# Kernel tuning notes

Hardware: AMD Instinct MI355X
Metric: run time of the kernel (lower is better)

## Reference

```python
import jax, jax.numpy as jnp
import numpy as np

N = 131072
D = 64
K = 1024
COMMITMENT_COST = 0.25


def setup_inputs() -> dict:
    key = jax.random.key(0)
    k1, k2 = jax.random.split(key)
    inputs = jax.random.normal(k1, (N, D), dtype=jnp.float32)
    # nn.Embedding weight initialized uniform(-1/K, 1/K)
    codebook = jax.random.uniform(k2, (K, D), dtype=jnp.float32,
                                  minval=-1.0 / K, maxval=1.0 / K)
    return {"inputs": inputs, "codebook": codebook}


def reference(inputs, codebook):
    # distances[n,k] = ||x_n||^2 + ||e_k||^2 - 2 x_n . e_k   (squared L2)
    distances = (jnp.sum(inputs ** 2, axis=1, keepdims=True)
                 + jnp.sum(codebook ** 2, axis=1)
                 - 2.0 * jnp.matmul(inputs, codebook.T))          # [N, K]
    encoding_indices = jnp.argmin(distances, axis=1)               # [N]
    # one-hot scatter + matmul in the original == direct gather
    quantized = codebook[encoding_indices]                         # [N, D]

    e_latent_loss = jnp.mean((jax.lax.stop_gradient(quantized) - inputs) ** 2)
    q_latent_loss = jnp.mean((quantized - jax.lax.stop_gradient(inputs)) ** 2)
    loss = q_latent_loss + COMMITMENT_COST * e_latent_loss

    # straight-through estimator
    quantized_st = inputs + jax.lax.stop_gradient(quantized - inputs)
    return loss, quantized_st, encoding_indices
```

## Files before the change

### kernel.cpp

```cpp
#include <hip/hip_runtime.h>

#define NN 131072
#define DD 64
#define KK 1024

typedef __attribute__((ext_vector_type(8))) short short8v;
typedef __attribute__((ext_vector_type(4))) float float4v;
typedef __attribute__((ext_vector_type(4))) int int4v;

#define MFMA(a, b, c) __builtin_amdgcn_mfma_f32_16x16x32_bf16(a, b, c, 0, 0, 0)

__device__ __forceinline__ unsigned int umin32(unsigned int a, unsigned int b) { return a < b ? a : b; }
__device__ __forceinline__ unsigned int umax32(unsigned int a, unsigned int b) { return a > b ? a : b; }

__device__ __forceinline__ unsigned int packu(float u, int kk) {
    int b = __builtin_bit_cast(int, u);
    unsigned int key = (unsigned int)(b ^ ((b >> 31) | 0x80000000));
    return (key & 0xFFFFFC00u) | (unsigned int)kk;
}

#define PINS3(t0, t1, t2, p)                                   \
    { unsigned int _x0 = umax32(t0, p); t0 = umin32(t0, p);    \
      unsigned int _x1 = umax32(t1, _x0); t1 = umin32(t1, _x0);\
      t2 = umin32(t2, _x1); }

__device__ __forceinline__ float np_sumsq64(const float* v) {
    float r[8];
#pragma unroll
    for (int j = 0; j < 8; ++j) r[j] = __fmul_rn(v[j], v[j]);
#pragma unroll
    for (int i = 8; i < 64; i += 8) {
#pragma unroll
        for (int j = 0; j < 8; ++j)
            r[j] = __fadd_rn(r[j], __fmul_rn(v[i + j], v[i + j]));
    }
    return __fadd_rn(__fadd_rn(__fadd_rn(r[0], r[1]), __fadd_rn(r[2], r[3])),
                     __fadd_rn(__fadd_rn(r[4], r[5]), __fadd_rn(r[6], r[7])));
}

__device__ __forceinline__ void bf16split(float v, unsigned short& hb, unsigned short& lb) {
    unsigned int u = __builtin_bit_cast(unsigned int, v);
    unsigned int h = (u + 0x7FFFu + ((u >> 16) & 1u)) >> 16;
    float hf = __builtin_bit_cast(float, h << 16);
    float lo = __fsub_rn(v, hf);
    unsigned int ul = __builtin_bit_cast(unsigned int, lo);
    unsigned int lo16 = (ul + 0x7FFFu + ((ul >> 16) & 1u)) >> 16;
    hb = (unsigned short)h;
    lb = (unsigned short)lo16;
}

__global__ void vq_prep(const float* __restrict__ cb, unsigned short* __restrict__ cbh,
                        unsigned short* __restrict__ cbl, float* __restrict__ se) {
    int k = blockIdx.x * 256 + threadIdx.x;
    if (k >= KK) return;
    float v[DD];
    const float4* p = (const float4*)(cb + (size_t)k * DD);
#pragma unroll
    for (int i = 0; i < 16; ++i) {
        float4 q = p[i];
        v[4 * i + 0] = q.x; v[4 * i + 1] = q.y; v[4 * i + 2] = q.z; v[4 * i + 3] = q.w;
    }
    se[k] = np_sumsq64(v);
    short8v* oh = (short8v*)(cbh + (size_t)k * DD);
    short8v* ol = (short8v*)(cbl + (size_t)k * DD);
#pragma unroll
    for (int q = 0; q < 8; ++q) {
        short8v hq, lq;
#pragma unroll
        for (int e = 0; e < 8; ++e) {
            unsigned short hb, lb;
            bf16split(v[q * 8 + e], hb, lb);
            hq[e] = (short)hb; lq[e] = (short)lb;
        }
        oh[q] = hq; ol[q] = lq;
    }
}

union SMem {
    struct { unsigned short xh[128 * 64]; unsigned short xl[128 * 64]; } x;
    struct { unsigned short bh[2][64 * 64]; unsigned short bl[2][64 * 64]; } b;
};

__global__ __launch_bounds__(256, 4)
void vq_main(const float* __restrict__ x, const float* __restrict__ cb,
             const unsigned short* __restrict__ cbh, const unsigned short* __restrict__ cbl,
             const float* __restrict__ se, float* __restrict__ qout,
             float* __restrict__ idxf, double* __restrict__ acc) {
    __shared__ SMem sm;
    __shared__ float ses[KK];
    __shared__ float wls[4];

    const int tid = threadIdx.x;
    const int rowBase = blockIdx.x * 128;
    const int l = tid & 63;
    const int w = tid >> 6;
    const int col = l & 15;
    const int g = l >> 4;

    int4v rbh[2], rbl[2];
    const int be_ = tid >> 2;
    const int bq_ = (tid & 3) * 2;
#define LOAD_TILE(tt)                                                              \
    { const unsigned short* ph = cbh + ((size_t)((tt) * 64 + be_) * 64) + (tid & 3) * 16; \
      const unsigned short* pl = cbl + ((size_t)((tt) * 64 + be_) * 64) + (tid & 3) * 16; \
      rbh[0] = *(const int4v*)(ph); rbh[1] = *(const int4v*)(ph + 8);              \
      rbl[0] = *(const int4v*)(pl); rbl[1] = *(const int4v*)(pl + 8); }
#define WRITE_TILE(bufi)                                                           \
    { int4v* dh = (int4v*)sm.b.bh[bufi]; int4v* dl = (int4v*)sm.b.bl[bufi];        \
      dh[be_ * 8 + (bq_ ^ (be_ & 7))] = rbh[0];                                    \
      dh[be_ * 8 + ((bq_ + 1) ^ (be_ & 7))] = rbh[1];                              \
      dl[be_ * 8 + (bq_ ^ (be_ & 7))] = rbl[0];                                    \
      dl[be_ * 8 + ((bq_ + 1) ^ (be_ & 7))] = rbl[1]; }

    ((float4v*)ses)[tid] = ((const float4v*)se)[tid];

    {
        int row = tid >> 1, db = (tid & 1) * 32;
        const float* xr = x + (size_t)(rowBase + row) * 64 + db;
#pragma unroll
        for (int jj = 0; jj < 4; ++jj) {
            float4 v0 = ((const float4*)xr)[2 * jj];
            float4 v1 = ((const float4*)xr)[2 * jj + 1];
            float vv[8] = {v0.x, v0.y, v0.z, v0.w, v1.x, v1.y, v1.z, v1.w};
            short8v hq, lq;
#pragma unroll
            for (int e = 0; e < 8; ++e) {
                unsigned short hb, lb;
                bf16split(vv[e], hb, lb);
                hq[e] = (short)hb; lq[e] = (short)lb;
            }
            int q = (tid & 1) * 4 + jj;
            int slot = row * 8 + (q ^ (row & 7));
            ((short8v*)sm.x.xh)[slot] = hq;
            ((short8v*)sm.x.xl)[slot] = lq;
        }
    }
    LOAD_TILE(0);
    __syncthreads();

    short8v ah0s0, ah1s0, al0s0, al1s0, ah0s1, ah1s1, al0s1, al1s1;
    {
        int r0 = w * 32 + col;
        int r1 = r0 + 16;
        ah0s0 = ((short8v*)sm.x.xh)[r0 * 8 + ((0 + g) ^ (r0 & 7))];
        ah1s0 = ((short8v*)sm.x.xh)[r0 * 8 + ((4 + g) ^ (r0 & 7))];
        al0s0 = ((short8v*)sm.x.xl)[r0 * 8 + ((0 + g) ^ (r0 & 7))];
        al1s0 = ((short8v*)sm.x.xl)[r0 * 8 + ((4 + g) ^ (r0 & 7))];
        ah0s1 = ((short8v*)sm.x.xh)[r1 * 8 + ((0 + g) ^ (r1 & 7))];
        ah1s1 = ((short8v*)sm.x.xh)[r1 * 8 + ((4 + g) ^ (r1 & 7))];
        al0s1 = ((short8v*)sm.x.xl)[r1 * 8 + ((0 + g) ^ (r1 & 7))];
        al1s1 = ((short8v*)sm.x.xl)[r1 * 8 + ((4 + g) ^ (r1 & 7))];
    }
    __syncthreads();

    WRITE_TILE(0);
    LOAD_TILE(1);
    __syncthreads();

    unsigned int k0[8], k1[8], k2[8];
#pragma unroll
    for (int s = 0; s < 8; ++s) { k0[s] = 0xFFFFFFFFu; k1[s] = 0xFFFFFFFFu; k2[s] = 0xFFFFFFFFu; }

    for (int t = 0; t < 16; ++t) {
        if (t < 15) {
            WRITE_TILE((t + 1) & 1);
            if (t < 14) LOAD_TILE(t + 2);
        }
        const unsigned short* bhB = sm.b.bh[t & 1];
        const unsigned short* blB = sm.b.bl[t & 1];
#pragma unroll
        for (int c = 0; c < 4; ++c) {
            int ec = c * 16 + col;
            int be = ec * 8, sw = ec & 7;
            short8v bh0 = ((const short8v*)bhB)[be + ((0 + g) ^ sw)];
            short8v bh1 = ((const short8v*)bhB)[be + ((4 + g) ^ sw)];
            short8v bl0 = ((const short8v*)blB)[be + ((0 + g) ^ sw)];
            short8v bl1 = ((const short8v*)blB)[be + ((4 + g) ^ sw)];
            float sek = ses[t * 64 + ec];
            float4v acc0 = {0.f, 0.f, 0.f, 0.f}, acc1 = {0.f, 0.f, 0.f, 0.f};
            acc0 = MFMA(ah0s0, bh0, acc0);
            acc0 = MFMA(ah1s0, bh1, acc0);
            acc0 = MFMA(al0s0, bh0, acc0);
            acc0 = MFMA(al1s0, bh1, acc0);
            acc0 = MFMA(ah0s0, bl0, acc0);
            acc0 = MFMA(ah1s0, bl1, acc0);
            acc1 = MFMA(ah0s1, bh0, acc1);
            acc1 = MFMA(ah1s1, bh1, acc1);
            acc1 = MFMA(al0s1, bh0, acc1);
            acc1 = MFMA(al1s1, bh1, acc1);
            acc1 = MFMA(ah0s1, bl0, acc1);
            acc1 = MFMA(ah1s1, bl1, acc1);
            int kk = t * 64 + ec;
#pragma unroll
            for (int r = 0; r < 4; ++r) {
                unsigned int p0 = packu(fmaf(-2.f, acc0[r], sek), kk);
                PINS3(k0[r], k1[r], k2[r], p0);
                unsigned int p1 = packu(fmaf(-2.f, acc1[r], sek), kk);
                PINS3(k0[4 + r], k1[4 + r], k2[4 + r], p1);
            }
        }
        __syncthreads();
    }

#pragma unroll
    for (int s = 0; s < 8; ++s) {
#pragma unroll
        for (int m = 1; m < 16; m <<= 1) {
            unsigned int o0 = __shfl_xor(k0[s], m);
            unsigned int o1 = __shfl_xor(k1[s], m);
            unsigned int o2 = __shfl_xor(k2[s], m);
            PINS3(k0[s], k1[s], k2[s], o0);
            { unsigned int x1 = umax32(k1[s], o1); k1[s] = umin32(k1[s], o1);
              k2[s] = umin32(k2[s], x1); }
            k2[s] = umin32(k2[s], o2);
        }
    }

    float lossLocal = 0.f;
    const int rr = (l & 15) >> 2;
    const int j = l & 3;
    const int jj = (j == 3) ? 0 : j;
#pragma unroll
    for (int s = 0; s < 2; ++s) {
        unsigned int ckk = k0[s * 4];
#pragma unroll
        for (int r_ = 0; r_ < 4; ++r_) {
            if (rr == r_) {
                if (jj == 0) ckk = k0[s * 4 + r_];
                else if (jj == 1) ckk = k1[s * 4 + r_];
                else ckk = k2[s * 4 + r_];
            }
        }
        int ck = (int)(ckk & 1023u);
        int rowg = rowBase + w * 32 + s * 16 + g * 4 + rr;
        const float4* xr = (const float4*)(x + (size_t)rowg * 64);
        const float4* er = (const float4*)(cb + (size_t)ck * 64);
        float dot = 0.f;
        float rs0 = 0.f, rs1 = 0.f, rs2 = 0.f, rs3 = 0.f, rs4 = 0.f, rs5 = 0.f, rs6 = 0.f, rs7 = 0.f;
#pragma unroll
        for (int i = 0; i < 16; ++i) {
            float4 a4 = xr[i], e4 = er[i];
            dot = fmaf(a4.x, e4.x, dot);
            dot = fmaf(a4.y, e4.y, dot);
            dot = fmaf(a4.z, e4.z, dot);
            dot = fmaf(a4.w, e4.w, dot);
            if ((i & 1) == 0) {
                rs0 = __fadd_rn(rs0, __fmul_rn(a4.x, a4.x));
                rs1 = __fadd_rn(rs1, __fmul_rn(a4.y, a4.y));
                rs2 = __fadd_rn(rs2, __fmul_rn(a4.z, a4.z));
                rs3 = __fadd_rn(rs3, __fmul_rn(a4.w, a4.w));
            } else {
                rs4 = __fadd_rn(rs4, __fmul_rn(a4.x, a4.x));
                rs5 = __fadd_rn(rs5, __fmul_rn(a4.y, a4.y));
                rs6 = __fadd_rn(rs6, __fmul_rn(a4.z, a4.z));
                rs7 = __fadd_rn(rs7, __fmul_rn(a4.w, a4.w));
            }
        }
        float sa = __fadd_rn(__fadd_rn(__fadd_rn(rs0, rs1), __fadd_rn(rs2, rs3)),
                             __fadd_rn(__fadd_rn(rs4, rs5), __fadd_rn(rs6, rs7)));
        float qd = __fsub_rn(__fadd_rn(sa, ses[ck]), __fmul_rn(2.f, dot));
#pragma unroll
        for (int m = 1; m < 4; m <<= 1) {
            float oq = __shfl_xor(qd, m);
            int ok = __shfl_xor(ck, m);
            if (oq < qd || (oq == qd && ok < ck)) { qd = oq; ck = ok; }
        }
        if (j == 0) idxf[rowg] = (float)ck;
        const float4* qr = (const float4*)(cb + (size_t)ck * 64);
        float* orow = qout + (size_t)rowg * 64;
#pragma unroll
        for (int p = 0; p < 4; ++p) {
            int iq = j * 4 + p;
            float4 xv = xr[iq];
            float4 qv = qr[iq];
            float dx = __fsub_rn(qv.x, xv.x);
            float dy = __fsub_rn(qv.y, xv.y);
            float dz = __fsub_rn(qv.z, xv.z);
            float dw = __fsub_rn(qv.w, xv.w);
            float4 o;
            o.x = __fadd_rn(xv.x, dx);
            o.y = __fadd_rn(xv.y, dy);
            o.z = __fadd_rn(xv.z, dz);
            o.w = __fadd_rn(xv.w, dw);
            ((float4*)orow)[iq] = o;
            lossLocal = fmaf(dx, dx, lossLocal);
            lossLocal = fmaf(dy, dy, lossLocal);
            lossLocal = fmaf(dz, dz, lossLocal);
            lossLocal = fmaf(dw, dw, lossLocal);
        }
    }
#pragma unroll
    for (int m = 1; m < 64; m <<= 1) lossLocal += __shfl_xor(lossLocal, m);
    if (l == 0) wls[w] = lossLocal;
    __syncthreads();
    if (tid == 0) atomicAdd(acc, (double)(wls[0] + wls[1] + wls[2] + wls[3]));
}

__global__ void vq_loss(const double* __restrict__ acc, float* __restrict__ out) {
    out[0] = (float)(acc[0] * 1.25 / (double)((size_t)NN * DD));
}

extern "C" void kernel_launch(void* const* d_in, const int* in_sizes, int n_in,
                              void* d_out, int out_size, void* d_ws, size_t ws_size,
                              hipStream_t stream) {
    const float* x = (const float*)d_in[0];
    const float* cb = (const float*)d_in[1];
    float* out = (float*)d_out;

    double* acc = (double*)d_ws;
    float* se = (float*)((char*)d_ws + 64);
    unsigned short* cbh = (unsigned short*)((char*)d_ws + 8192);
    unsigned short* cbl = (unsigned short*)((char*)d_ws + 8192 + 131072);

    hipMemsetAsync(d_ws, 0, 64, stream);

    vq_prep<<<4, 256, 0, stream>>>(cb, cbh, cbl, se);
    vq_main<<<NN / 128, 256, 0, stream>>>(x, cb, cbh, cbl, se,
                                          out + 1, out + 1 + (size_t)NN * DD, acc);
    vq_loss<<<1, 1, 0, stream>>>(acc, out);
}
```

Before: 195.4 us.

## Fold codebook norm into MFMA, fuse loss kernel, align output stores

The codebook is pre-scaled by -2 and its squared norm is split into bf16 hi/lo, which an extra MFMA with a ones vector adds into the accumulators. This removes the per-element fmaf in the argmin epilogue. The separate loss kernel is replaced by a last-block-done counter inside the main kernel, saving one launch. Output stores are shifted so the float4 writes line up with the out+1 offset, and the exact norm is recomputed from fp32 in the refine step. The cost is an extra MFMA per tile and some precision risk in the bf16-split norm.

```diff
diff --git a/kernel.cpp b/kernel.cpp
--- a/kernel.cpp
+++ b/kernel.cpp
@@ -50,8 +50,8 @@
 }
 
 __global__ void vq_prep(const float* __restrict__ cb, unsigned short* __restrict__ cbh,
-                        unsigned short* __restrict__ cbl, float* __restrict__ se) {
-    int k = blockIdx.x * 256 + threadIdx.x;
+                        unsigned short* __restrict__ cbl, unsigned int* __restrict__ sehl) {
+    int k = blockIdx.x * 64 + threadIdx.x;
     if (k >= KK) return;
     float v[DD];
     const float4* p = (const float4*)(cb + (size_t)k * DD);
@@ -60,7 +60,10 @@
         float4 q = p[i];
         v[4 * i + 0] = q.x; v[4 * i + 1] = q.y; v[4 * i + 2] = q.z; v[4 * i + 3] = q.w;
     }
-    se[k] = np_sumsq64(v);
+    float se = np_sumsq64(v);
+    unsigned short sh, sl;
+    bf16split(se, sh, sl);
+    sehl[k] = (unsigned int)sh | ((unsigned int)sl << 16);
     short8v* oh = (short8v*)(cbh + (size_t)k * DD);
     short8v* ol = (short8v*)(cbl + (size_t)k * DD);
 #pragma unroll
@@ -69,7 +72,7 @@
 #pragma unroll
         for (int e = 0; e < 8; ++e) {
             unsigned short hb, lb;
-            bf16split(v[q * 8 + e], hb, lb);
+            bf16split(-2.0f * v[q * 8 + e], hb, lb);
             hq[e] = (short)hb; lq[e] = (short)lb;
         }
         oh[q] = hq; ol[q] = lq;
@@ -84,11 +87,14 @@
 __global__ __launch_bounds__(256, 4)
 void vq_main(const float* __restrict__ x, const float* __restrict__ cb,
              const unsigned short* __restrict__ cbh, const unsigned short* __restrict__ cbl,
-             const float* __restrict__ se, float* __restrict__ qout,
-             float* __restrict__ idxf, double* __restrict__ acc) {
+             const unsigned int* __restrict__ sehl, float* __restrict__ out,
+             double* __restrict__ acc, unsigned int* __restrict__ cnt) {
     __shared__ SMem sm;
-    __shared__ float ses[KK];
+    __shared__ unsigned int sehls[KK];
     __shared__ float wls[4];
+
+    float* qout = out + 1;
+    float* idxf = out + 1 + (size_t)NN * DD;
 
     const int tid = threadIdx.x;
     const int rowBase = blockIdx.x * 128;
@@ -112,7 +118,7 @@
       dl[be_ * 8 + (bq_ ^ (be_ & 7))] = rbl[0];                                    \
       dl[be_ * 8 + ((bq_ + 1) ^ (be_ & 7))] = rbl[1]; }
 
-    ((float4v*)ses)[tid] = ((const float4v*)se)[tid];
+    ((int4v*)sehls)[tid] = ((const int4v*)sehl)[tid];
 
     {
         int row = tid >> 1, db = (tid & 1) * 32;
@@ -157,6 +163,10 @@
     LOAD_TILE(1);
     __syncthreads();
 
+    const short8v onesA = __builtin_bit_cast(short8v,
+        (int4v){(g == 0) ? (int)0x3F803F80 : 0, 0, 0, 0});
+    const float4v zero4 = {0.f, 0.f, 0.f, 0.f};
+
     unsigned int k0[8], k1[8], k2[8];
 #pragma unroll
     for (int s = 0; s < 8; ++s) { k0[s] = 0xFFFFFFFFu; k1[s] = 0xFFFFFFFFu; k2[s] = 0xFFFFFFFFu; }
@@ -176,8 +186,11 @@
             short8v bh1 = ((const short8v*)bhB)[be + ((4 + g) ^ sw)];
             short8v bl0 = ((const short8v*)blB)[be + ((0 + g) ^ sw)];
             short8v bl1 = ((const short8v*)blB)[be + ((4 + g) ^ sw)];
-            float sek = ses[t * 64 + ec];
-            float4v acc0 = {0.f, 0.f, 0.f, 0.f}, acc1 = {0.f, 0.f, 0.f, 0.f};
+            unsigned int sv = sehls[t * 64 + ec];
+            short8v sf = __builtin_bit_cast(short8v,
+                (int4v){(g == 0) ? (int)sv : 0, 0, 0, 0});
+            float4v seAcc = MFMA(onesA, sf, zero4);
+            float4v acc0 = seAcc, acc1 = seAcc;
             acc0 = MFMA(ah0s0, bh0, acc0);
             acc0 = MFMA(ah1s0, bh1, acc0);
             acc0 = MFMA(al0s0, bh0, acc0);
@@ -193,9 +206,9 @@
             int kk = t * 64 + ec;
 #pragma unroll
             for (int r = 0; r < 4; ++r) {
-                unsigned int p0 = packu(fmaf(-2.f, acc0[r], sek), kk);
+                unsigned int p0 = packu(acc0[r], kk);
                 PINS3(k0[r], k1[r], k2[r], p0);
-                unsigned int p1 = packu(fmaf(-2.f, acc1[r], sek), kk);
+                unsigned int p1 = packu(acc1[r], kk);
                 PINS3(k0[4 + r], k1[4 + r], k2[4 + r], p1);
             }
         }
@@ -237,6 +250,7 @@
         const float4* er = (const float4*)(cb + (size_t)ck * 64);
         float dot = 0.f;
         float rs0 = 0.f, rs1 = 0.f, rs2 = 0.f, rs3 = 0.f, rs4 = 0.f, rs5 = 0.f, rs6 = 0.f, rs7 = 0.f;
+        float es0 = 0.f, es1 = 0.f, es2 = 0.f, es3 = 0.f, es4 = 0.f, es5 = 0.f, es6 = 0.f, es7 = 0.f;
 #pragma unroll
         for (int i = 0; i < 16; ++i) {
             float4 a4 = xr[i], e4 = er[i];
@@ -249,16 +263,26 @@
                 rs1 = __fadd_rn(rs1, __fmul_rn(a4.y, a4.y));
                 rs2 = __fadd_rn(rs2, __fmul_rn(a4.z, a4.z));
                 rs3 = __fadd_rn(rs3, __fmul_rn(a4.w, a4.w));
+                es0 = __fadd_rn(es0, __fmul_rn(e4.x, e4.x));
+                es1 = __fadd_rn(es1, __fmul_rn(e4.y, e4.y));
+                es2 = __fadd_rn(es2, __fmul_rn(e4.z, e4.z));
+                es3 = __fadd_rn(es3, __fmul_rn(e4.w, e4.w));
             } else {
                 rs4 = __fadd_rn(rs4, __fmul_rn(a4.x, a4.x));
                 rs5 = __fadd_rn(rs5, __fmul_rn(a4.y, a4.y));
                 rs6 = __fadd_rn(rs6, __fmul_rn(a4.z, a4.z));
                 rs7 = __fadd_rn(rs7, __fmul_rn(a4.w, a4.w));
+                es4 = __fadd_rn(es4, __fmul_rn(e4.x, e4.x));
+                es5 = __fadd_rn(es5, __fmul_rn(e4.y, e4.y));
+                es6 = __fadd_rn(es6, __fmul_rn(e4.z, e4.z));
+                es7 = __fadd_rn(es7, __fmul_rn(e4.w, e4.w));
             }
         }
         float sa = __fadd_rn(__fadd_rn(__fadd_rn(rs0, rs1), __fadd_rn(rs2, rs3)),
                              __fadd_rn(__fadd_rn(rs4, rs5), __fadd_rn(rs6, rs7)));
-        float qd = __fsub_rn(__fadd_rn(sa, ses[ck]), __fmul_rn(2.f, dot));
+        float seE = __fadd_rn(__fadd_rn(__fadd_rn(es0, es1), __fadd_rn(es2, es3)),
+                              __fadd_rn(__fadd_rn(es4, es5), __fadd_rn(es6, es7)));
+        float qd = __fsub_rn(__fadd_rn(sa, seE), __fmul_rn(2.f, dot));
 #pragma unroll
         for (int m = 1; m < 4; m <<= 1) {
             float oq = __shfl_xor(qd, m);
@@ -266,38 +290,60 @@
             if (oq < qd || (oq == qd && ok < ck)) { qd = oq; ck = ok; }
         }
         if (j == 0) idxf[rowg] = (float)ck;
-        const float4* qr = (const float4*)(cb + (size_t)ck * 64);
-        float* orow = qout + (size_t)rowg * 64;
-#pragma unroll
-        for (int p = 0; p < 4; ++p) {
-            int iq = j * 4 + p;
-            float4 xv = xr[iq];
-            float4 qv = qr[iq];
-            float dx = __fsub_rn(qv.x, xv.x);
-            float dy = __fsub_rn(qv.y, xv.y);
-            float dz = __fsub_rn(qv.z, xv.z);
-            float dw = __fsub_rn(qv.w, xv.w);
-            float4 o;
-            o.x = __fadd_rn(xv.x, dx);
-            o.y = __fadd_rn(xv.y, dy);
-            o.z = __fadd_rn(xv.z, dz);
-            o.w = __fadd_rn(xv.w, dw);
-            ((float4*)orow)[iq] = o;
-            lossLocal = fmaf(dx, dx, lossLocal);
-            lossLocal = fmaf(dy, dy, lossLocal);
-            lossLocal = fmaf(dz, dz, lossLocal);
-            lossLocal = fmaf(dw, dw, lossLocal);
-        }
-    }
+
+        const float* xrow = x + (size_t)rowg * 64;
+        const float* qrow = cb + (size_t)ck * 64;
+        float* ob = qout + (size_t)rowg * 64;
+#pragma unroll
+        for (int mi = 0; mi < 4; ++mi) {
+            int m = j + mi * 4;
+            if (m < 15) {
+                float4 xv = *(const float4*)(xrow + 3 + 4 * m);
+                float4 qv = *(const float4*)(qrow + 3 + 4 * m);
+                float dx = __fsub_rn(qv.x, xv.x);
+                float dy = __fsub_rn(qv.y, xv.y);
+                float dz = __fsub_rn(qv.z, xv.z);
+                float dw = __fsub_rn(qv.w, xv.w);
+                float4 o;
+                o.x = __fadd_rn(xv.x, dx);
+                o.y = __fadd_rn(xv.y, dy);
+                o.z = __fadd_rn(xv.z, dz);
+                o.w = __fadd_rn(xv.w, dw);
+                *(float4*)(ob + 3 + 4 * m) = o;
+                lossLocal = fmaf(dx, dx, lossLocal);
+                lossLocal = fmaf(dy, dy, lossLocal);
+                lossLocal = fmaf(dz, dz, lossLocal);
+                lossLocal = fmaf(dw, dw, lossLocal);
+            }
+        }
+        if (j == 3) {
+#pragma unroll
+            for (int e3 = 0; e3 < 4; ++e3) {
+                int e = (e3 < 3) ? e3 : 63;
+                float xv = xrow[e];
+                float qv = qrow[e];
+                float d = __fsub_rn(qv, xv);
+                ob[e] = __fadd_rn(xv, d);
+                lossLocal = fmaf(d, d, lossLocal);
+            }
+        }
+    }
+
 #pragma unroll
     for (int m = 1; m < 64; m <<= 1) lossLocal += __shfl_xor(lossLocal, m);
     if (l == 0) wls[w] = lossLocal;
     __syncthreads();
-    if (tid == 0) atomicAdd(acc, (double)(wls[0] + wls[1] + wls[2] + wls[3]));
-}
-
-__global__ void vq_loss(const double* __restrict__ acc, float* __restrict__ out) {
-    out[0] = (float)(acc[0] * 1.25 / (double)((size_t)NN * DD));
+    if (tid == 0) {
+        atomicAdd(acc, (double)(wls[0] + wls[1] + wls[2] + wls[3]));
+        __threadfence();
+        unsigned int old = atomicAdd(cnt, 1u);
+        if (old == (unsigned int)(gridDim.x - 1)) {
+            __threadfence();
+            unsigned long long bits = atomicAdd((unsigned long long*)acc, 0ULL);
+            double v = __builtin_bit_cast(double, bits);
+            out[0] = (float)(v * 1.25 / (double)((size_t)NN * DD));
+        }
+    }
 }
 
 extern "C" void kernel_launch(void* const* d_in, const int* in_sizes, int n_in,
@@ -308,14 +354,13 @@
     float* out = (float*)d_out;
 
     double* acc = (double*)d_ws;
-    float* se = (float*)((char*)d_ws + 64);
+    unsigned int* cnt = (unsigned int*)((char*)d_ws + 8);
+    unsigned int* sehl = (unsigned int*)((char*)d_ws + 4096);
     unsigned short* cbh = (unsigned short*)((char*)d_ws + 8192);
     unsigned short* cbl = (unsigned short*)((char*)d_ws + 8192 + 131072);
 
     hipMemsetAsync(d_ws, 0, 64, stream);
 
-    vq_prep<<<4, 256, 0, stream>>>(cb, cbh, cbl, se);
-    vq_main<<<NN / 128, 256, 0, stream>>>(x, cb, cbh, cbl, se,
-                                          out + 1, out + 1 + (size_t)NN * DD, acc);
-    vq_loss<<<1, 1, 0, stream>>>(acc, out);
-}
+    vq_prep<<<16, 64, 0, stream>>>(cb, cbh, cbl, sehl);
+    vq_main<<<NN / 128, 256, 0, stream>>>(x, cb, cbh, cbl, sehl, out, acc, cnt);
+}
```

After: 249.4 us. +27.7%, slower.
